# Kernel optimization log

Hardware: AMD Instinct MI355X
Metric: run time of the kernel (lower is better)

The kernel has to match this reference:

```python
import jax, jax.numpy as jnp
import numpy as np

TEMPERATURE = 0.5
EPS = 1e-8  # torch F.cosine_similarity norm clamp


def setup_inputs() -> dict:
    key = jax.random.key(0)
    k1, k2 = jax.random.split(key)
    N, D = 4096, 256
    z1 = jax.random.normal(k1, (N, D), dtype=jnp.float32)
    z2 = jax.random.normal(k2, (N, D), dtype=jnp.float32)
    return {"z1": z1, "z2": z2}


def _l2norm(x):
    # matches torch cosine_similarity eps clamping on the norm
    n = jnp.sqrt(jnp.sum(x * x, axis=-1, keepdims=True))
    return x / jnp.maximum(n, EPS)


def reference(z1, z2):
    N = z1.shape[0]
    f = jnp.concatenate([z1, z2], axis=0)          # [2N, D]
    fn = _l2norm(f)                                 # row-normalized
    sim = fn @ fn.T                                 # [2N, 2N] cosine similarities
    diag = jnp.eye(2 * N, dtype=bool)
    # denominator: sum over off-diagonal entries (self-similarity excluded)
    denom = jnp.sum(jnp.where(diag, 0.0, jnp.exp(sim / TEMPERATURE)), axis=1)  # [2N]
    # positives: cosine(z1_i, z2_i), duplicated for both views
    z1n, z2n = _l2norm(z1), _l2norm(z2)
    pos = jnp.sum(z1n * z2n, axis=1)               # [N]
    pos = jnp.concatenate([pos, pos], axis=0)      # [2N]
    loss = -jnp.mean(jnp.log(jnp.exp(pos / TEMPERATURE) / denom))
    return loss
```

## Files before the change

### kernel.cpp

```cpp
#include <hip/hip_runtime.h>

#define D 256
#define SCALE 1.69864354f
#define EPS 1e-8f

typedef __attribute__((ext_vector_type(8))) __bf16 bf16x8;
typedef __attribute__((ext_vector_type(4))) __bf16 bf16x4;
typedef __attribute__((ext_vector_type(4))) float  f32x4;

__global__ __launch_bounds__(256) void normpos_kernel(
    const float* __restrict__ z1, const float* __restrict__ z2,
    __bf16* __restrict__ fn, float* __restrict__ pos, int N) {
  int wid  = threadIdx.x >> 6;
  int lane = threadIdx.x & 63;
  int row  = blockIdx.x * 4 + wid;
  f32x4 a = *(const f32x4*)(z1 + (size_t)row * D + lane * 4);
  f32x4 b = *(const f32x4*)(z2 + (size_t)row * D + lane * 4);
  float s1  = a.x * a.x + a.y * a.y + a.z * a.z + a.w * a.w;
  float s2  = b.x * b.x + b.y * b.y + b.z * b.z + b.w * b.w;
  float dot = a.x * b.x + a.y * b.y + a.z * b.z + a.w * b.w;
  #pragma unroll
  for (int m = 1; m < 64; m <<= 1) {
    s1  += __shfl_xor(s1, m, 64);
    s2  += __shfl_xor(s2, m, 64);
    dot += __shfl_xor(dot, m, 64);
  }
  float inv1 = 1.0f / fmaxf(sqrtf(s1), EPS);
  float inv2 = 1.0f / fmaxf(sqrtf(s2), EPS);
  float q1 = inv1 * SCALE, q2 = inv2 * SCALE;
  bf16x4 o1, o2;
  o1[0] = (__bf16)(a.x * q1); o1[1] = (__bf16)(a.y * q1);
  o1[2] = (__bf16)(a.z * q1); o1[3] = (__bf16)(a.w * q1);
  o2[0] = (__bf16)(b.x * q2); o2[1] = (__bf16)(b.y * q2);
  o2[2] = (__bf16)(b.z * q2); o2[3] = (__bf16)(b.w * q2);
  *(bf16x4*)(fn + (size_t)row * D + lane * 4)       = o1;
  *(bf16x4*)(fn + (size_t)(N + row) * D + lane * 4) = o2;
  if (lane == 0) pos[row] = dot * inv1 * inv2;
}


__device__ __forceinline__ void stage_tile(const __bf16* __restrict__ row0,
                                           int kk, __bf16* lds, int tid) {
  #pragma unroll
  for (int it = 0; it < 4; ++it) {
    int s = it * 256 + tid;
    int r = s >> 3;
    int p = s & 7;
    const __bf16* src = row0 + (size_t)r * D + kk * 64 + ((p ^ (r & 7)) << 3);
    __builtin_amdgcn_global_load_lds(
        (const __attribute__((address_space(1))) void*)src,
        (__attribute__((address_space(3))) void*)(lds + s * 8), 16, 0, 0);
  }
}

__global__ __launch_bounds__(256, 4) void denom_kernel(
    const __bf16* __restrict__ fn, float* __restrict__ partial, int twoN) {
  __shared__ __bf16 As[128 * 64];
  __shared__ __bf16 Bs[128 * 64];
  __shared__ float  redsumR[128][2];
  __shared__ float  redsumC[128][2];

  int tid  = threadIdx.x;
  int wid  = tid >> 6;
  int lane = tid & 63;
  int c = lane & 15;
  int g = lane >> 4;
  int wr = wid >> 1, wc = wid & 1;

  int bid = blockIdx.x;
  int i = (int)((sqrtf(8.f * (float)bid + 1.f) - 1.f) * 0.5f);
  while ((i + 1) * (i + 2) / 2 <= bid) ++i;
  while (i * (i + 1) / 2 > bid) --i;
  int rb = bid - i * (i + 1) / 2;
  int cb = i;
  const __bf16* Arow0 = fn + (size_t)rb * 128 * D;
  const __bf16* Brow0 = fn + (size_t)cb * 128 * D;

  bool dblk  = (rb == cb);
  bool dwave = dblk && (wr == wc);

  f32x4 acc[4][4] = {};

  stage_tile(Arow0, 0, As, tid);
  stage_tile(Brow0, 0, Bs, tid);

  #pragma unroll
  for (int kk = 0; kk < 4; ++kk) {
    __syncthreads();
    #pragma unroll
    for (int ks = 0; ks < 2; ++ks) {
      bf16x8 a[4], b[4];
      #pragma unroll
      for (int mi = 0; mi < 4; ++mi) {
        int ar = wr * 64 + mi * 16 + c;
        a[mi] = *(const bf16x8*)((const char*)As + ar * 128 +
                                 ((((ks << 2) + g) ^ (ar & 7)) << 4));
      }
      #pragma unroll
      for (int ni = 0; ni < 4; ++ni) {
        int bc = wc * 64 + ni * 16 + c;
        b[ni] = *(const bf16x8*)((const char*)Bs + bc * 128 +
                                 ((((ks << 2) + g) ^ (bc & 7)) << 4));
      }
      #pragma unroll
      for (int mi = 0; mi < 4; ++mi)
        #pragma unroll
        for (int ni = 0; ni < 4; ++ni)
          acc[mi][ni] = __builtin_amdgcn_mfma_f32_16x16x32_bf16(
              a[mi], b[ni], acc[mi][ni], 0, 0, 0);
    }
    if (kk < 3) {
      __syncthreads();
      stage_tile(Arow0, kk + 1, As, tid);
      stage_tile(Brow0, kk + 1, Bs, tid);
    }
  }

  float rsum[16];
  float csum[4];
  #pragma unroll
  for (int ii = 0; ii < 16; ++ii) rsum[ii] = 0.f;
  #pragma unroll
  for (int ii = 0; ii < 4; ++ii) csum[ii] = 0.f;

  if (dwave) {
    #pragma unroll
    for (int mi = 0; mi < 4; ++mi)
      #pragma unroll
      for (int ni = 0; ni < 4; ++ni) {
        int colloc = ni * 16 + c;
        #pragma unroll
        for (int r = 0; r < 4; ++r) {
          int rowloc = mi * 16 + g * 4 + r;
          float e = __builtin_amdgcn_exp2f(acc[mi][ni][r]);
          if (rowloc == colloc) e = 0.f;
          rsum[mi * 4 + r] += e;
        }
      }
  } else if (dblk) {
    #pragma unroll
    for (int mi = 0; mi < 4; ++mi)
      #pragma unroll
      for (int ni = 0; ni < 4; ++ni)
        #pragma unroll
        for (int r = 0; r < 4; ++r)
          rsum[mi * 4 + r] += __builtin_amdgcn_exp2f(acc[mi][ni][r]);
  } else {
    #pragma unroll
    for (int mi = 0; mi < 4; ++mi)
      #pragma unroll
      for (int ni = 0; ni < 4; ++ni)
        #pragma unroll
        for (int r = 0; r < 4; ++r) {
          float e = __builtin_amdgcn_exp2f(acc[mi][ni][r]);
          rsum[mi * 4 + r] += e;
          csum[ni]         += e;
        }
  }

  #pragma unroll
  for (int ii = 0; ii < 16; ++ii) {
    float v = rsum[ii];
    v += __shfl_xor(v, 1, 64);
    v += __shfl_xor(v, 2, 64);
    v += __shfl_xor(v, 4, 64);
    v += __shfl_xor(v, 8, 64);
    rsum[ii] = v;
  }
  if (c == 0) {
    #pragma unroll
    for (int mi = 0; mi < 4; ++mi)
      #pragma unroll
      for (int r = 0; r < 4; ++r)
        redsumR[wr * 64 + mi * 16 + g * 4 + r][wc] = rsum[mi * 4 + r];
  }
  if (!dblk) {
    #pragma unroll
    for (int ii = 0; ii < 4; ++ii) {
      float v = csum[ii];
      v += __shfl_xor(v, 16, 64);
      v += __shfl_xor(v, 32, 64);
      csum[ii] = v;
    }
    if (g == 0) {
      #pragma unroll
      for (int ni = 0; ni < 4; ++ni)
        redsumC[wc * 64 + ni * 16 + c][wr] = csum[ni];
    }
  }
  __syncthreads();
  if (tid < 128) {
    partial[(size_t)cb * twoN + rb * 128 + tid] =
        redsumR[tid][0] + redsumR[tid][1];
    if (rb != cb)
      partial[(size_t)rb * twoN + cb * 128 + tid] =
          redsumC[tid][0] + redsumC[tid][1];
  }
}

__global__ __launch_bounds__(256) void reduce1_kernel(
    const float* __restrict__ partial, const float* __restrict__ pos,
    float* __restrict__ bsum, int twoN, int N, int nsplit) {
  int row = blockIdx.x * 256 + threadIdx.x;
  int wid = threadIdx.x >> 6, lane = threadIdx.x & 63;
  float denom = 0.f;
  for (int s = 0; s < nsplit; ++s) denom += partial[(size_t)s * twoN + row];
  float ld = logf(denom);
  float p  = (row < N) ? pos[row] : 0.f;
  #pragma unroll
  for (int m = 1; m < 64; m <<= 1) {
    ld += __shfl_xor(ld, m, 64);
    p  += __shfl_xor(p, m, 64);
  }
  __shared__ float sld[4], spo[4];
  if (lane == 0) { sld[wid] = ld; spo[wid] = p; }
  __syncthreads();
  if (threadIdx.x == 0) {
    bsum[blockIdx.x]      = sld[0] + sld[1] + sld[2] + sld[3];
    bsum[32 + blockIdx.x] = spo[0] + spo[1] + spo[2] + spo[3];
  }
}

__global__ void reduce2_kernel(const float* __restrict__ bsum,
                               float* __restrict__ out, int twoN, int N,
                               int nblk) {
  int t = threadIdx.x;
  float ld = (t < nblk) ? bsum[t] : 0.f;
  float p  = (t < nblk) ? bsum[32 + t] : 0.f;
  #pragma unroll
  for (int m = 1; m < 64; m <<= 1) {
    ld += __shfl_xor(ld, m, 64);
    p  += __shfl_xor(p, m, 64);
  }
  if (t == 0) out[0] = ld / (float)twoN - 2.f * (p / (float)N);
}

extern "C" void kernel_launch(void* const* d_in, const int* in_sizes, int n_in,
                              void* d_out, int out_size, void* d_ws,
                              size_t ws_size, hipStream_t stream) {
  const float* z1 = (const float*)d_in[0];
  const float* z2 = (const float*)d_in[1];
  int N = in_sizes[0] / D;
  int twoN = 2 * N;
  int nrb = twoN / 128;

  __bf16* fn      = (__bf16*)d_ws;
  float*  partial = (float*)((char*)d_ws + (size_t)twoN * D * 2);
  float*  pos     = (float*)((char*)partial + (size_t)nrb * twoN * 4);
  float*  bsum    = (float*)((char*)pos + (size_t)N * 4);

  normpos_kernel<<<N / 4, 256, 0, stream>>>(z1, z2, fn, pos, N);
  int ntri = nrb * (nrb + 1) / 2;
  denom_kernel<<<ntri, 256, 0, stream>>>(fn, partial, twoN);
  int nblk = twoN / 256;
  reduce1_kernel<<<nblk, 256, 0, stream>>>(partial, pos, bsum, twoN, N, nrb);
  reduce2_kernel<<<1, 64, 0, stream>>>(bsum, (float*)d_out, twoN, N, nblk);
}
```

Before: 60.74 us.

## Restructure symmetric sim tiling: 256-row strips with register-resident A and double-buffered B

The denominator kernel now gives each block a 256-row strip and a 256-column chunk of the upper triangle (528 blocks). Each wave keeps its 64 rows of A fully in registers across the whole K=256, and streams 64-column B tiles through double-buffered LDS with full-K staging. This cuts the number of barriers and A reloads compared with the old 128x128 tiles that staged K in 64-wide slices. Column sums are written per 64-column subtile, and the reduce kernel reads the new partial layout. The cost is higher register use (occupancy 2) and hardcoded sizes (528 blocks, 32 row blocks) that assume N=4096.

```diff
diff --git a/kernel.cpp b/kernel.cpp
--- a/kernel.cpp
+++ b/kernel.cpp
@@ -39,125 +39,140 @@
 }
 
 
-__device__ __forceinline__ void stage_tile(const __bf16* __restrict__ row0,
-                                           int kk, __bf16* lds, int tid) {
-  #pragma unroll
-  for (int it = 0; it < 4; ++it) {
-    int s = it * 256 + tid;
-    int r = s >> 3;
-    int p = s & 7;
-    const __bf16* src = row0 + (size_t)r * D + kk * 64 + ((p ^ (r & 7)) << 3);
+__device__ __forceinline__ void stageB(const __bf16* __restrict__ fn,
+                                       int colg0, __bf16* lds, int tid) {
+  #pragma unroll
+  for (int it = 0; it < 8; ++it) {
+    int s   = it * 256 + tid;
+    int col = s >> 5;
+    int p   = s & 31;
+    const __bf16* src =
+        fn + (size_t)(colg0 + col) * D + ((p ^ (col & 7)) << 3);
     __builtin_amdgcn_global_load_lds(
         (const __attribute__((address_space(1))) void*)src,
         (__attribute__((address_space(3))) void*)(lds + s * 8), 16, 0, 0);
   }
 }
 
-__global__ __launch_bounds__(256, 4) void denom_kernel(
+__global__ __launch_bounds__(256, 2) void denom_kernel(
     const __bf16* __restrict__ fn, float* __restrict__ partial, int twoN) {
-  __shared__ __bf16 As[128 * 64];
-  __shared__ __bf16 Bs[128 * 64];
-  __shared__ float  redsumR[128][2];
-  __shared__ float  redsumC[128][2];
+  __shared__ __bf16 Bs[2][64 * 256];
+  __shared__ float  redC[2][64][4];
 
   int tid  = threadIdx.x;
   int wid  = tid >> 6;
   int lane = tid & 63;
   int c = lane & 15;
   int g = lane >> 4;
-  int wr = wid >> 1, wc = wid & 1;
 
   int bid = blockIdx.x;
-  int i = (int)((sqrtf(8.f * (float)bid + 1.f) - 1.f) * 0.5f);
-  while ((i + 1) * (i + 2) / 2 <= bid) ++i;
-  while (i * (i + 1) / 2 > bid) --i;
-  int rb = bid - i * (i + 1) / 2;
-  int cb = i;
-  const __bf16* Arow0 = fn + (size_t)rb * 128 * D;
-  const __bf16* Brow0 = fn + (size_t)cb * 128 * D;
-
-  bool dblk  = (rb == cb);
-  bool dwave = dblk && (wr == wc);
-
-  f32x4 acc[4][4] = {};
-
-  stage_tile(Arow0, 0, As, tid);
-  stage_tile(Brow0, 0, Bs, tid);
-
-  #pragma unroll
-  for (int kk = 0; kk < 4; ++kk) {
+  int rb = (int)((65.f - sqrtf(65.f * 65.f - 8.f * (float)bid)) * 0.5f);
+  while ((rb + 1) * (65 - (rb + 1)) / 2 <= bid) ++rb;
+  while (rb * (65 - rb) / 2 > bid) --rb;
+  int chunk = bid - rb * (65 - rb) / 2;
+  int rowbase = rb * 256 + wid * 64;
+  int colg0   = rb * 256 + chunk * 256;
+  bool diagchunk = (chunk == 0);
+
+  stageB(fn, colg0, Bs[0], tid);
+
+  bf16x8 a[4][8];
+  #pragma unroll
+  for (int mi = 0; mi < 4; ++mi)
+    #pragma unroll
+    for (int ks = 0; ks < 8; ++ks)
+      a[mi][ks] = *(const bf16x8*)(fn + (size_t)(rowbase + mi * 16 + c) * D +
+                                   ks * 32 + g * 8);
+
+  float rsum[16];
+  #pragma unroll
+  for (int ii = 0; ii < 16; ++ii) rsum[ii] = 0.f;
+
+  #pragma unroll
+  for (int t = 0; t < 4; ++t) {
+    int cur = t & 1;
     __syncthreads();
+    if (t < 3) stageB(fn, colg0 + (t + 1) * 64, Bs[cur ^ 1], tid);
+    if (!diagchunk && t > 0 && tid < 64) {
+      float v = redC[cur ^ 1][tid][0] + redC[cur ^ 1][tid][1] +
+                redC[cur ^ 1][tid][2] + redC[cur ^ 1][tid][3];
+      partial[(size_t)rb * twoN + colg0 + (t - 1) * 64 + tid] = v;
+    }
+    f32x4 acc[4][4] = {};
     #pragma unroll
-    for (int ks = 0; ks < 2; ++ks) {
-      bf16x8 a[4], b[4];
-      #pragma unroll
-      for (int mi = 0; mi < 4; ++mi) {
-        int ar = wr * 64 + mi * 16 + c;
-        a[mi] = *(const bf16x8*)((const char*)As + ar * 128 +
-                                 ((((ks << 2) + g) ^ (ar & 7)) << 4));
-      }
+    for (int ks = 0; ks < 8; ++ks) {
+      bf16x8 b[4];
       #pragma unroll
       for (int ni = 0; ni < 4; ++ni) {
-        int bc = wc * 64 + ni * 16 + c;
-        b[ni] = *(const bf16x8*)((const char*)Bs + bc * 128 +
-                                 ((((ks << 2) + g) ^ (bc & 7)) << 4));
+        int col = ni * 16 + c;
+        b[ni] = *(const bf16x8*)((const char*)Bs[cur] + col * 512 +
+                                 (((ks * 4 + g) ^ (col & 7)) << 4));
       }
       #pragma unroll
       for (int mi = 0; mi < 4; ++mi)
         #pragma unroll
         for (int ni = 0; ni < 4; ++ni)
           acc[mi][ni] = __builtin_amdgcn_mfma_f32_16x16x32_bf16(
-              a[mi], b[ni], acc[mi][ni], 0, 0, 0);
-    }
-    if (kk < 3) {
-      __syncthreads();
-      stage_tile(Arow0, kk + 1, As, tid);
-      stage_tile(Brow0, kk + 1, Bs, tid);
-    }
-  }
-
-  float rsum[16];
-  float csum[4];
-  #pragma unroll
-  for (int ii = 0; ii < 16; ++ii) rsum[ii] = 0.f;
-  #pragma unroll
-  for (int ii = 0; ii < 4; ++ii) csum[ii] = 0.f;
-
-  if (dwave) {
-    #pragma unroll
-    for (int mi = 0; mi < 4; ++mi)
+              a[mi][ks], b[ni], acc[mi][ni], 0, 0, 0);
+    }
+    if (diagchunk) {
+      if (t == wid) {
+        #pragma unroll
+        for (int mi = 0; mi < 4; ++mi)
+          #pragma unroll
+          for (int ni = 0; ni < 4; ++ni) {
+            int colloc = ni * 16 + c;
+            #pragma unroll
+            for (int r = 0; r < 4; ++r) {
+              int rowloc = mi * 16 + g * 4 + r;
+              float e = __builtin_amdgcn_exp2f(acc[mi][ni][r]);
+              if (rowloc == colloc) e = 0.f;
+              rsum[mi * 4 + r] += e;
+            }
+          }
+      } else {
+        #pragma unroll
+        for (int mi = 0; mi < 4; ++mi)
+          #pragma unroll
+          for (int ni = 0; ni < 4; ++ni)
+            #pragma unroll
+            for (int r = 0; r < 4; ++r)
+              rsum[mi * 4 + r] += __builtin_amdgcn_exp2f(acc[mi][ni][r]);
+      }
+    } else {
+      float csum[4] = {0.f, 0.f, 0.f, 0.f};
+      #pragma unroll
+      for (int mi = 0; mi < 4; ++mi)
+        #pragma unroll
+        for (int ni = 0; ni < 4; ++ni)
+          #pragma unroll
+          for (int r = 0; r < 4; ++r) {
+            float e = __builtin_amdgcn_exp2f(acc[mi][ni][r]);
+            rsum[mi * 4 + r] += e;
+            csum[ni]         += e;
+          }
       #pragma unroll
       for (int ni = 0; ni < 4; ++ni) {
-        int colloc = ni * 16 + c;
-        #pragma unroll
-        for (int r = 0; r < 4; ++r) {
-          int rowloc = mi * 16 + g * 4 + r;
-          float e = __builtin_amdgcn_exp2f(acc[mi][ni][r]);
-          if (rowloc == colloc) e = 0.f;
-          rsum[mi * 4 + r] += e;
-        }
-      }
-  } else if (dblk) {
-    #pragma unroll
-    for (int mi = 0; mi < 4; ++mi)
-      #pragma unroll
-      for (int ni = 0; ni < 4; ++ni)
-        #pragma unroll
-        for (int r = 0; r < 4; ++r)
-          rsum[mi * 4 + r] += __builtin_amdgcn_exp2f(acc[mi][ni][r]);
-  } else {
-    #pragma unroll
-    for (int mi = 0; mi < 4; ++mi)
-      #pragma unroll
-      for (int ni = 0; ni < 4; ++ni)
-        #pragma unroll
-        for (int r = 0; r < 4; ++r) {
-          float e = __builtin_amdgcn_exp2f(acc[mi][ni][r]);
-          rsum[mi * 4 + r] += e;
-          csum[ni]         += e;
-        }
-  }
-
+        float v = csum[ni];
+        v += __shfl_xor(v, 16, 64);
+        v += __shfl_xor(v, 32, 64);
+        csum[ni] = v;
+      }
+      if (g == 0) {
+        #pragma unroll
+        for (int ni = 0; ni < 4; ++ni)
+          redC[cur][ni * 16 + c][wid] = csum[ni];
+      }
+    }
+  }
+  if (!diagchunk) {
+    __syncthreads();
+    if (tid < 64) {
+      float v = redC[1][tid][0] + redC[1][tid][1] +
+                redC[1][tid][2] + redC[1][tid][3];
+      partial[(size_t)rb * twoN + colg0 + 3 * 64 + tid] = v;
+    }
+  }
   #pragma unroll
   for (int ii = 0; ii < 16; ++ii) {
     float v = rsum[ii];
@@ -168,43 +183,26 @@
     rsum[ii] = v;
   }
   if (c == 0) {
+    float* dst = partial + (size_t)(32 + rb + chunk) * twoN + rowbase;
     #pragma unroll
-    for (int mi = 0; mi < 4; ++mi)
-      #pragma unroll
-      for (int r = 0; r < 4; ++r)
-        redsumR[wr * 64 + mi * 16 + g * 4 + r][wc] = rsum[mi * 4 + r];
-  }
-  if (!dblk) {
-    #pragma unroll
-    for (int ii = 0; ii < 4; ++ii) {
-      float v = csum[ii];
-      v += __shfl_xor(v, 16, 64);
-      v += __shfl_xor(v, 32, 64);
-      csum[ii] = v;
-    }
-    if (g == 0) {
-      #pragma unroll
-      for (int ni = 0; ni < 4; ++ni)
-        redsumC[wc * 64 + ni * 16 + c][wr] = csum[ni];
-    }
-  }
-  __syncthreads();
-  if (tid < 128) {
-    partial[(size_t)cb * twoN + rb * 128 + tid] =
-        redsumR[tid][0] + redsumR[tid][1];
-    if (rb != cb)
-      partial[(size_t)rb * twoN + cb * 128 + tid] =
-          redsumC[tid][0] + redsumC[tid][1];
+    for (int mi = 0; mi < 4; ++mi) {
+      f32x4 v;
+      v.x = rsum[mi * 4 + 0]; v.y = rsum[mi * 4 + 1];
+      v.z = rsum[mi * 4 + 2]; v.w = rsum[mi * 4 + 3];
+      *(f32x4*)(dst + mi * 16 + g * 4) = v;
+    }
   }
 }
 
 __global__ __launch_bounds__(256) void reduce1_kernel(
     const float* __restrict__ partial, const float* __restrict__ pos,
-    float* __restrict__ bsum, int twoN, int N, int nsplit) {
-  int row = blockIdx.x * 256 + threadIdx.x;
+    float* __restrict__ bsum, int twoN, int N) {
+  int rbi = blockIdx.x;
+  int row = rbi * 256 + threadIdx.x;
   int wid = threadIdx.x >> 6, lane = threadIdx.x & 63;
   float denom = 0.f;
-  for (int s = 0; s < nsplit; ++s) denom += partial[(size_t)s * twoN + row];
+  for (int s = 0; s < rbi; ++s)    denom += partial[(size_t)s * twoN + row];
+  for (int q = rbi; q < 32; ++q)   denom += partial[(size_t)(32 + q) * twoN + row];
   float ld = logf(denom);
   float p  = (row < N) ? pos[row] : 0.f;
   #pragma unroll
@@ -242,17 +240,14 @@
   const float* z2 = (const float*)d_in[1];
   int N = in_sizes[0] / D;
   int twoN = 2 * N;
-  int nrb = twoN / 128;
 
   __bf16* fn      = (__bf16*)d_ws;
   float*  partial = (float*)((char*)d_ws + (size_t)twoN * D * 2);
-  float*  pos     = (float*)((char*)partial + (size_t)nrb * twoN * 4);
+  float*  pos     = (float*)((char*)partial + (size_t)64 * twoN * 4);
   float*  bsum    = (float*)((char*)pos + (size_t)N * 4);
 
   normpos_kernel<<<N / 4, 256, 0, stream>>>(z1, z2, fn, pos, N);
-  int ntri = nrb * (nrb + 1) / 2;
-  denom_kernel<<<ntri, 256, 0, stream>>>(fn, partial, twoN);
-  int nblk = twoN / 256;
-  reduce1_kernel<<<nblk, 256, 0, stream>>>(partial, pos, bsum, twoN, N, nrb);
-  reduce2_kernel<<<1, 64, 0, stream>>>(bsum, (float*)d_out, twoN, N, nblk);
-}
+  denom_kernel<<<528, 256, 0, stream>>>(fn, partial, twoN);
+  reduce1_kernel<<<32, 256, 0, stream>>>(partial, pos, bsum, twoN, N);
+  reduce2_kernel<<<1, 64, 0, stream>>>(bsum, (float*)d_out, twoN, N, 32);
+}
```

New measurement: 66.08 us. 1.09x slower.
